# Kernel optimization log

Hardware: AMD Instinct MI355X
Metric: run time of the kernel (lower is better)

Reference implementation:

```python
import jax, jax.numpy as jnp
import numpy as np

B, N, D, R = 4, 50000, 64, 500
E_PER = 62500
E = B * E_PER


def _build_edges():
    rng = np.random.default_rng(0)
    idx = np.repeat(np.arange(B), E_PER)
    vi = rng.integers(0, N, E)
    vj = rng.integers(0, N, E)
    order = np.lexsort((vj, vi, idx))
    idx, vi, vj = idx[order], vi[order], vj[order]
    rel = rng.integers(0, R, E)
    key_vi = idx.astype(np.int64) * N + vi
    _, idx_vi = np.unique(key_vi, return_inverse=True)  # sorted -> nondecreasing segment ids
    key_vj = idx.astype(np.int64) * N + vj
    _, idx_vj = np.unique(key_vj, return_inverse=True)
    all_keys = np.concatenate([key_vi, key_vj])
    uniq_all, inv = np.unique(all_keys, return_inverse=True)
    e2vi, e2vj = inv[:E], inv[E:]
    sel = np.stack([idx, vi, vj, rel, idx_vi, idx_vj, e2vi, e2vj], axis=1).astype(np.int32)
    return sel, int(idx_vi.max() + 1), int(idx_vj.max() + 1), int(len(uniq_all))


def setup_inputs() -> dict:
    sel, n_vi_seg, n_vj_seg, n_visited = _build_edges()
    key = jax.random.key(0)
    ks = jax.random.split(key, 9)
    na = jax.random.uniform(ks[0], (B, N), jnp.float32) + 1e-6
    na = na / jnp.sum(na, axis=1, keepdims=True)
    return {
        'node_attention': na,
        'selected_edges': jnp.asarray(sel),
        'edges_y': jax.random.uniform(ks[1], (E,), jnp.float32, 0.1, 1.0),
        'hidden_con': jax.random.normal(ks[2], (n_visited, D), jnp.float32) * 0.1,
        'hidden_uncon': jax.random.normal(ks[3], (1, N, D), jnp.float32) * 0.1,
        'rel_emb': jax.random.normal(ks[4], (R, D), jnp.float32) * 0.1,
        'ws': jax.random.normal(ks[5], (8, D), jnp.float32) * (1.0 / np.sqrt(8.0)),
        'b': jax.random.normal(ks[6], (D,), jnp.float32) * 0.01,
        'out_w': jax.random.normal(ks[7], (D,), jnp.float32) * 0.3,
        'out_b': jax.random.normal(ks[8], (D,), jnp.float32) * 0.01,
        'n_vi_seg': n_vi_seg,
        'n_vj_seg': n_vj_seg,
    }


def reference(node_attention, selected_edges, edges_y, hidden_con, hidden_uncon,
              rel_emb, ws, b, out_w, out_b, n_vi_seg, n_vj_seg):
    idx, vi, vj = selected_edges[:, 0], selected_edges[:, 1], selected_edges[:, 2]
    rel, idx_vi, idx_vj = selected_edges[:, 3], selected_edges[:, 4], selected_edges[:, 5]
    e2vi, e2vj = selected_edges[:, 6], selected_edges[:, 7]

    # Node2Edge gathers
    hc_vi, hc_vj = hidden_con[e2vi], hidden_con[e2vj]        # [E, D]
    hu = hidden_uncon[0]                                     # hidden_uncon has batch 1
    hu_vi, hu_vj = hu[vi], hu[vj]                            # [E, D]
    re = rel_emb[rel]                                        # [E, D]

    # F layer: interact = [[0,3],[0,2,3],[0,4],[0,2,4],[1,3],[1,2,3],[1,4],[1,2,4]]
    terms = (hc_vi * hc_vj, hc_vi * re * hc_vj, hc_vi * hu_vj, hc_vi * re * hu_vj,
             hu_vi * hc_vj, hu_vi * re * hc_vj, hu_vi * hu_vj, hu_vi * re * hu_vj)
    f = b
    for k in range(8):
        f = f + ws[k] * terms[k]
    f = jax.nn.relu(f) * out_w + out_b                       # [E, D]
    logits = jnp.sum(f, axis=1)                              # [E]

    # NeighborSoftmax at='vi' (segment softmax)
    seg_max = jax.ops.segment_max(logits, idx_vi, num_segments=n_vi_seg)
    e = jnp.exp(logits - seg_max[idx_vi])
    es = jax.ops.segment_sum(e, idx_vi, num_segments=n_vi_seg)
    transition = e / es[idx_vi]

    # attention flow
    na_e = node_attention[idx, vi]
    ta = na_e * transition * edges_y

    # Aggregate at='vj', sum, then scatter into (B, n_nodes)
    aggr = jax.ops.segment_sum(ta, idx_vj, num_segments=n_vj_seg)
    seg_idx = jax.ops.segment_max(idx, idx_vj, num_segments=n_vj_seg)
    seg_vj = jax.ops.segment_max(vj, idx_vj, num_segments=n_vj_seg)
    Bn, Nn = node_attention.shape
    new_att = jnp.zeros((Bn, Nn), node_attention.dtype).at[seg_idx, seg_vj].add(aggr)
    return new_att / jnp.sum(new_att, axis=1, keepdims=True)
```

## Files before the change

kernel.cpp:

```cpp
#include <hip/hip_runtime.h>
#include <math.h>

#define D 64
#define CH 256
#define HALO 32
#define WSZ (CH + HALO)
#define BT 512
#define NT ((WSZ + 63) / 64)

__global__ void k_zero(float4* __restrict__ out4, float* __restrict__ row_sum,
                       int BN4, int Bn)
{
    const int i = blockIdx.x * 256 + threadIdx.x;
    if (i < BN4) out4[i] = make_float4(0.f, 0.f, 0.f, 0.f);
    if (i < Bn) row_sum[i] = 0.f;
}

__device__ __forceinline__ float edge_logit(
    const float4 a, const float4 c, const float4 ui, const float4 uj,
    const float4 r, const float* Wf, const float* Bvf, const float* Owf)
{
    const float* ap = (const float*)&a;  const float* cp = (const float*)&c;
    const float* up = (const float*)&ui; const float* vp = (const float*)&uj;
    const float* rp = (const float*)&r;
    float acc = 0.f;
    #pragma unroll
    for (int k4 = 0; k4 < 4; ++k4) {
        const float hcvi = ap[k4], hcvj = cp[k4], huvi = up[k4], huvj = vp[k4], rr = rp[k4];
        const float hcr = hcvi * rr, hur = huvi * rr;
        float f = Bvf[k4];
        f += Wf[0*4+k4] * (hcvi * hcvj);
        f += Wf[1*4+k4] * (hcr  * hcvj);
        f += Wf[2*4+k4] * (hcvi * huvj);
        f += Wf[3*4+k4] * (hcr  * huvj);
        f += Wf[4*4+k4] * (huvi * hcvj);
        f += Wf[5*4+k4] * (hur  * hcvj);
        f += Wf[6*4+k4] * (huvi * huvj);
        f += Wf[7*4+k4] * (hur  * huvj);
        acc += fmaxf(f, 0.f) * Owf[k4];
    }
    return acc;
}

#define ISSUE(A0, UI0, R0, A1, UI1, R1, C0, UJ0, C1, UJ1, T)              \
    {                                                                     \
        const int jj0 = (T) * 64 + wv * 8 + g;                            \
        const int jj1 = jj0 + 4;                                          \
        const int jc0 = (jj0 < Wc) ? jj0 : (Wc - 1);                      \
        const int jc1 = (jj1 < Wc) ? jj1 : (Wc - 1);                      \
        A0  = hc4[(size_t)s_sel[jc0 * 8 + 6] * 16 + d16];                 \
        UI0 = hu4[(size_t)s_sel[jc0 * 8 + 1] * 16 + d16];                 \
        R0  = re4[(size_t)s_sel[jc0 * 8 + 3] * 16 + d16];                 \
        C0  = hc4[(size_t)s_sel[jc0 * 8 + 7] * 16 + d16];                 \
        UJ0 = hu4[(size_t)s_sel[jc0 * 8 + 2] * 16 + d16];                 \
        A1  = hc4[(size_t)s_sel[jc1 * 8 + 6] * 16 + d16];                 \
        UI1 = hu4[(size_t)s_sel[jc1 * 8 + 1] * 16 + d16];                 \
        R1  = re4[(size_t)s_sel[jc1 * 8 + 3] * 16 + d16];                 \
        C1  = hc4[(size_t)s_sel[jc1 * 8 + 7] * 16 + d16];                 \
        UJ1 = hu4[(size_t)s_sel[jc1 * 8 + 2] * 16 + d16];                 \
    }

#define COMPUTE(A0, UI0, R0, A1, UI1, R1, C0, UJ0, C1, UJ1, T)            \
    {                                                                     \
        const int jj0 = (T) * 64 + wv * 8 + g;                            \
        const int jj1 = jj0 + 4;                                          \
        const bool v0 = (jj0 < Wc);                                       \
        const bool v1 = (jj1 < Wc);                                       \
        const int jc0 = v0 ? jj0 : (Wc - 1);                              \
        const int jc1 = v1 ? jj1 : (Wc - 1);                              \
        float acc0 = edge_logit(A0, C0, UI0, UJ0, R0, Wf, Bvf, Owf);      \
        float acc1 = edge_logit(A1, C1, UI1, UJ1, R1, Wf, Bvf, Owf);      \
        _Pragma("unroll")                                                 \
        for (int off = 8; off > 0; off >>= 1) {                           \
            acc0 += __shfl_xor(acc0, off, 64);                            \
            acc1 += __shfl_xor(acc1, off, 64);                            \
        }                                                                 \
        if (d16 == 0) {                                                   \
            if (v0) { s_logit[jj0] = acc0; s_ivi[jj0] = s_sel[jc0 * 8 + 4]; } \
            if (v1) { s_logit[jj1] = acc1; s_ivi[jj1] = s_sel[jc1 * 8 + 4]; } \
        }                                                                 \
    }

#define SCHED_FENCE() __builtin_amdgcn_sched_barrier(0)

__global__ __launch_bounds__(BT) void k_fused(
    const int* __restrict__ sel, const float* __restrict__ hc,
    const float* __restrict__ hu, const float* __restrict__ re,
    const float* __restrict__ wsm, const float* __restrict__ bias,
    const float* __restrict__ out_w,
    const float* __restrict__ na, const float* __restrict__ edges_y,
    float* __restrict__ out, float* __restrict__ row_sum,
    int E, int N)
{
    __shared__ int   s_sel[WSZ * 8];
    __shared__ float s_logit[WSZ];
    __shared__ int   s_ivi[WSZ];
    __shared__ float s_row[8];

    const int b0 = blockIdx.x * CH;
    const int Wc = min(WSZ, E - b0);

    {
        const int nint = Wc * 8;
        const int* selw = sel + (size_t)b0 * 8;
        for (int i = threadIdx.x; i < nint; i += BT) s_sel[i] = selw[i];
    }
    if (threadIdx.x < 8) s_row[threadIdx.x] = 0.f;

    const int lane = threadIdx.x & 63;
    const int g    = lane >> 4;
    const int d16  = lane & 15;
    const int wv   = threadIdx.x >> 6;

    const float4* wsm4 = (const float4*)wsm;
    float4 Wk[8];
    #pragma unroll
    for (int k = 0; k < 8; ++k) Wk[k] = wsm4[k * 16 + d16];
    const float4 Bv = ((const float4*)bias)[d16];
    const float4 Ow = ((const float4*)out_w)[d16];
    const float* Wf  = (const float*)Wk;
    const float* Bvf = (const float*)&Bv;
    const float* Owf = (const float*)&Ow;

    const float4* hc4 = (const float4*)hc;
    const float4* hu4 = (const float4*)hu;
    const float4* re4 = (const float4*)re;

    __syncthreads();

    float4 nA0a, nUI0a, nR0a, nA1a, nUI1a, nR1a, fC0a, fUJ0a, fC1a, fUJ1a;
    float4 nA0b, nUI0b, nR0b, nA1b, nUI1b, nR1b, fC0b, fUJ0b, fC1b, fUJ1b;

    ISSUE(nA0a, nUI0a, nR0a, nA1a, nUI1a, nR1a, fC0a, fUJ0a, fC1a, fUJ1a, 0);
    SCHED_FENCE();

    int t = 0;
    #pragma unroll 1
    for (; t + 1 < NT; t += 2) {
        ISSUE(nA0b, nUI0b, nR0b, nA1b, nUI1b, nR1b, fC0b, fUJ0b, fC1b, fUJ1b, t + 1);
        SCHED_FENCE();
        COMPUTE(nA0a, nUI0a, nR0a, nA1a, nUI1a, nR1a, fC0a, fUJ0a, fC1a, fUJ1a, t);
        SCHED_FENCE();
        ISSUE(nA0a, nUI0a, nR0a, nA1a, nUI1a, nR1a, fC0a, fUJ0a, fC1a, fUJ1a, t + 2);
        SCHED_FENCE();
        COMPUTE(nA0b, nUI0b, nR0b, nA1b, nUI1b, nR1b, fC0b, fUJ0b, fC1b, fUJ1b, t + 1);
        SCHED_FENCE();
    }
    COMPUTE(nA0a, nUI0a, nR0a, nA1a, nUI1a, nR1a, fC0a, fUJ0a, fC1a, fUJ1a, NT - 1);

    __syncthreads();

    const int ivi_prev = (b0 > 0) ? sel[((size_t)b0 - 1) * 8 + 4] : -1;

    for (int j = threadIdx.x; j < Wc; j += BT) {
        const int myivi = s_ivi[j];

        int s = j;
        while (s > 0 && s_ivi[s - 1] == myivi) --s;
        const bool genuine = (s > 0) || (myivi != ivi_prev);
        if (!genuine || s >= CH) continue;

        int en = j + 1;
        while (en < Wc && s_ivi[en] == myivi) ++en;

        float m = s_logit[j];
        for (int i = s; i < en; ++i) m = fmaxf(m, s_logit[i]);
        float sum = 0.f;
        for (int i = s; i < en; ++i) sum += __expf(s_logit[i] - m);

        const int idx = s_sel[j * 8 + 0];
        const int vi  = s_sel[j * 8 + 1];
        const int vj  = s_sel[j * 8 + 2];
        const float ta = na[(size_t)idx * N + vi]
                       * (__expf(s_logit[j] - m) / sum) * edges_y[b0 + j];

        atomicAdd(out + (size_t)idx * N + vj, ta);
        atomicAdd(&s_row[idx & 7], ta);
    }

    __syncthreads();
    if (threadIdx.x < 8) {
        const float v = s_row[threadIdx.x];
        if (v != 0.f) atomicAdd(row_sum + threadIdx.x, v);
    }
}

__global__ void k_norm(float4* __restrict__ out, const float* __restrict__ row_sum, int N4) {
    const int col = blockIdx.x * blockDim.x + threadIdx.x;
    const int row = blockIdx.y;
    if (col < N4) {
        const float inv = 1.f / row_sum[row];
        const size_t i = (size_t)row * N4 + col;
        float4 v = out[i];
        v.x *= inv; v.y *= inv; v.z *= inv; v.w *= inv;
        out[i] = v;
    }
}

extern "C" void kernel_launch(void* const* d_in, const int* in_sizes, int n_in,
                              void* d_out, int out_size, void* d_ws, size_t ws_size,
                              hipStream_t stream)
{
    const float* na    = (const float*)d_in[0];
    const int*   sel   = (const int*)  d_in[1];
    const float* ey    = (const float*)d_in[2];
    const float* hc    = (const float*)d_in[3];
    const float* hu    = (const float*)d_in[4];
    const float* re    = (const float*)d_in[5];
    const float* wsm   = (const float*)d_in[6];
    const float* bias  = (const float*)d_in[7];
    const float* ow    = (const float*)d_in[8];

    float* out = (float*)d_out;

    const int E  = in_sizes[2];
    const int N  = in_sizes[4] / D;
    const int BN = in_sizes[0];
    const int Bn = BN / N;

    float* row_sum = (float*)d_ws;

    const int N4  = N / 4;
    const int BN4 = BN / 4;

    k_zero<<<(BN4 + 255) / 256, 256, 0, stream>>>((float4*)out, row_sum, BN4, Bn);

    const int nblk = (E + CH - 1) / CH;
    k_fused<<<nblk, BT, 0, stream>>>(sel, hc, hu, re, wsm, bias, ow,
                                     na, ey, out, row_sum, E, N);

    dim3 ngrid((N4 + 255) / 256, Bn);
    k_norm<<<ngrid, 256, 0, stream>>>((float4*)out, row_sum, N4);
}
```

Baseline: 159.7 us.

## Simplify edge loop, move weights to shared memory, shrink block and chunk

Removes the hand-pipelined double-buffered gather (ISSUE/COMPUTE with scheduling barriers). Each wave now processes one edge per 16-lane group per iteration and the weight, bias and out_w vectors are read from LDS instead of registers. Chunk size drops from 256 to 128 edges and block size from 512 to 256 threads, which lowers register pressure so more waves can be resident to hide gather latency. In exchange it loses explicit load/compute overlap and doubles the halo overhead relative to the chunk size.

```diff
diff --git a/kernel.cpp b/kernel.cpp
--- a/kernel.cpp
+++ b/kernel.cpp
@@ -2,11 +2,11 @@
 #include <math.h>
 
 #define D 64
-#define CH 256
+#define CH 128
 #define HALO 32
 #define WSZ (CH + HALO)
-#define BT 512
-#define NT ((WSZ + 63) / 64)
+#define BT 256
+#define NT (WSZ / 16)
 
 __global__ void k_zero(float4* __restrict__ out4, float* __restrict__ row_sum,
                        int BN4, int Bn)
@@ -15,73 +15,6 @@
     if (i < BN4) out4[i] = make_float4(0.f, 0.f, 0.f, 0.f);
     if (i < Bn) row_sum[i] = 0.f;
 }
-
-__device__ __forceinline__ float edge_logit(
-    const float4 a, const float4 c, const float4 ui, const float4 uj,
-    const float4 r, const float* Wf, const float* Bvf, const float* Owf)
-{
-    const float* ap = (const float*)&a;  const float* cp = (const float*)&c;
-    const float* up = (const float*)&ui; const float* vp = (const float*)&uj;
-    const float* rp = (const float*)&r;
-    float acc = 0.f;
-    #pragma unroll
-    for (int k4 = 0; k4 < 4; ++k4) {
-        const float hcvi = ap[k4], hcvj = cp[k4], huvi = up[k4], huvj = vp[k4], rr = rp[k4];
-        const float hcr = hcvi * rr, hur = huvi * rr;
-        float f = Bvf[k4];
-        f += Wf[0*4+k4] * (hcvi * hcvj);
-        f += Wf[1*4+k4] * (hcr  * hcvj);
-        f += Wf[2*4+k4] * (hcvi * huvj);
-        f += Wf[3*4+k4] * (hcr  * huvj);
-        f += Wf[4*4+k4] * (huvi * hcvj);
-        f += Wf[5*4+k4] * (hur  * hcvj);
-        f += Wf[6*4+k4] * (huvi * huvj);
-        f += Wf[7*4+k4] * (hur  * huvj);
-        acc += fmaxf(f, 0.f) * Owf[k4];
-    }
-    return acc;
-}
-
-#define ISSUE(A0, UI0, R0, A1, UI1, R1, C0, UJ0, C1, UJ1, T)              \
-    {                                                                     \
-        const int jj0 = (T) * 64 + wv * 8 + g;                            \
-        const int jj1 = jj0 + 4;                                          \
-        const int jc0 = (jj0 < Wc) ? jj0 : (Wc - 1);                      \
-        const int jc1 = (jj1 < Wc) ? jj1 : (Wc - 1);                      \
-        A0  = hc4[(size_t)s_sel[jc0 * 8 + 6] * 16 + d16];                 \
-        UI0 = hu4[(size_t)s_sel[jc0 * 8 + 1] * 16 + d16];                 \
-        R0  = re4[(size_t)s_sel[jc0 * 8 + 3] * 16 + d16];                 \
-        C0  = hc4[(size_t)s_sel[jc0 * 8 + 7] * 16 + d16];                 \
-        UJ0 = hu4[(size_t)s_sel[jc0 * 8 + 2] * 16 + d16];                 \
-        A1  = hc4[(size_t)s_sel[jc1 * 8 + 6] * 16 + d16];                 \
-        UI1 = hu4[(size_t)s_sel[jc1 * 8 + 1] * 16 + d16];                 \
-        R1  = re4[(size_t)s_sel[jc1 * 8 + 3] * 16 + d16];                 \
-        C1  = hc4[(size_t)s_sel[jc1 * 8 + 7] * 16 + d16];                 \
-        UJ1 = hu4[(size_t)s_sel[jc1 * 8 + 2] * 16 + d16];                 \
-    }
-
-#define COMPUTE(A0, UI0, R0, A1, UI1, R1, C0, UJ0, C1, UJ1, T)            \
-    {                                                                     \
-        const int jj0 = (T) * 64 + wv * 8 + g;                            \
-        const int jj1 = jj0 + 4;                                          \
-        const bool v0 = (jj0 < Wc);                                       \
-        const bool v1 = (jj1 < Wc);                                       \
-        const int jc0 = v0 ? jj0 : (Wc - 1);                              \
-        const int jc1 = v1 ? jj1 : (Wc - 1);                              \
-        float acc0 = edge_logit(A0, C0, UI0, UJ0, R0, Wf, Bvf, Owf);      \
-        float acc1 = edge_logit(A1, C1, UI1, UJ1, R1, Wf, Bvf, Owf);      \
-        _Pragma("unroll")                                                 \
-        for (int off = 8; off > 0; off >>= 1) {                           \
-            acc0 += __shfl_xor(acc0, off, 64);                            \
-            acc1 += __shfl_xor(acc1, off, 64);                            \
-        }                                                                 \
-        if (d16 == 0) {                                                   \
-            if (v0) { s_logit[jj0] = acc0; s_ivi[jj0] = s_sel[jc0 * 8 + 4]; } \
-            if (v1) { s_logit[jj1] = acc1; s_ivi[jj1] = s_sel[jc1 * 8 + 4]; } \
-        }                                                                 \
-    }
-
-#define SCHED_FENCE() __builtin_amdgcn_sched_barrier(0)
 
 __global__ __launch_bounds__(BT) void k_fused(
     const int* __restrict__ sel, const float* __restrict__ hc,
@@ -95,6 +28,9 @@
     __shared__ int   s_sel[WSZ * 8];
     __shared__ float s_logit[WSZ];
     __shared__ int   s_ivi[WSZ];
+    __shared__ float s_w[8 * D];
+    __shared__ float s_bv[D];
+    __shared__ float s_ow[D];
     __shared__ float s_row[8];
 
     const int b0 = blockIdx.x * CH;
@@ -104,23 +40,18 @@
         const int nint = Wc * 8;
         const int* selw = sel + (size_t)b0 * 8;
         for (int i = threadIdx.x; i < nint; i += BT) s_sel[i] = selw[i];
+        for (int i = threadIdx.x; i < 8 * D; i += BT) s_w[i] = wsm[i];
+        if (threadIdx.x < D) {
+            s_bv[threadIdx.x] = bias[threadIdx.x];
+            s_ow[threadIdx.x] = out_w[threadIdx.x];
+        }
+        if (threadIdx.x < 8) s_row[threadIdx.x] = 0.f;
     }
-    if (threadIdx.x < 8) s_row[threadIdx.x] = 0.f;
 
     const int lane = threadIdx.x & 63;
     const int g    = lane >> 4;
     const int d16  = lane & 15;
     const int wv   = threadIdx.x >> 6;
-
-    const float4* wsm4 = (const float4*)wsm;
-    float4 Wk[8];
-    #pragma unroll
-    for (int k = 0; k < 8; ++k) Wk[k] = wsm4[k * 16 + d16];
-    const float4 Bv = ((const float4*)bias)[d16];
-    const float4 Ow = ((const float4*)out_w)[d16];
-    const float* Wf  = (const float*)Wk;
-    const float* Bvf = (const float*)&Bv;
-    const float* Owf = (const float*)&Ow;
 
     const float4* hc4 = (const float4*)hc;
     const float4* hu4 = (const float4*)hu;
@@ -128,25 +59,52 @@
 
     __syncthreads();
 
-    float4 nA0a, nUI0a, nR0a, nA1a, nUI1a, nR1a, fC0a, fUJ0a, fC1a, fUJ1a;
-    float4 nA0b, nUI0b, nR0b, nA1b, nUI1b, nR1b, fC0b, fUJ0b, fC1b, fUJ1b;
+    #pragma unroll 1
+    for (int t = 0; t < NT; ++t) {
+        const int jj = t * 16 + wv * 4 + g;
+        const bool v = (jj < Wc);
+        const int jc = v ? jj : (Wc - 1);
 
-    ISSUE(nA0a, nUI0a, nR0a, nA1a, nUI1a, nR1a, fC0a, fUJ0a, fC1a, fUJ1a, 0);
-    SCHED_FENCE();
+        const int e2vi = s_sel[jc * 8 + 6];
+        const int vig  = s_sel[jc * 8 + 1];
+        const int rel  = s_sel[jc * 8 + 3];
+        const int e2vj = s_sel[jc * 8 + 7];
+        const int vjg  = s_sel[jc * 8 + 2];
 
-    int t = 0;
-    #pragma unroll 1
-    for (; t + 1 < NT; t += 2) {
-        ISSUE(nA0b, nUI0b, nR0b, nA1b, nUI1b, nR1b, fC0b, fUJ0b, fC1b, fUJ1b, t + 1);
-        SCHED_FENCE();
-        COMPUTE(nA0a, nUI0a, nR0a, nA1a, nUI1a, nR1a, fC0a, fUJ0a, fC1a, fUJ1a, t);
-        SCHED_FENCE();
-        ISSUE(nA0a, nUI0a, nR0a, nA1a, nUI1a, nR1a, fC0a, fUJ0a, fC1a, fUJ1a, t + 2);
-        SCHED_FENCE();
-        COMPUTE(nA0b, nUI0b, nR0b, nA1b, nUI1b, nR1b, fC0b, fUJ0b, fC1b, fUJ1b, t + 1);
-        SCHED_FENCE();
+        const float4 a  = hc4[(size_t)e2vi * 16 + d16];
+        const float4 ui = hu4[(size_t)vig  * 16 + d16];
+        const float4 r  = re4[(size_t)rel  * 16 + d16];
+        const float4 c  = hc4[(size_t)e2vj * 16 + d16];
+        const float4 uj = hu4[(size_t)vjg  * 16 + d16];
+
+        float4 ar, uir;
+        ar.x  = a.x  * r.x;  ar.y  = a.y  * r.y;  ar.z  = a.z  * r.z;  ar.w  = a.w  * r.w;
+        uir.x = ui.x * r.x;  uir.y = ui.y * r.y;  uir.z = ui.z * r.z;  uir.w = ui.w * r.w;
+
+        float4 f = *(const float4*)(s_bv + (d16 << 2));
+        #pragma unroll
+        for (int k = 0; k < 8; ++k) {
+            const float4 w = *(const float4*)(s_w + k * D + (d16 << 2));
+            const float4 p = (k & 4) ? ((k & 1) ? uir : ui) : ((k & 1) ? ar : a);
+            const float4 q = (k & 2) ? uj : c;
+            f.x += w.x * (p.x * q.x);
+            f.y += w.y * (p.y * q.y);
+            f.z += w.z * (p.z * q.z);
+            f.w += w.w * (p.w * q.w);
+        }
+        const float4 ow = *(const float4*)(s_ow + (d16 << 2));
+        float acc = fmaxf(f.x, 0.f) * ow.x + fmaxf(f.y, 0.f) * ow.y
+                  + fmaxf(f.z, 0.f) * ow.z + fmaxf(f.w, 0.f) * ow.w;
+
+        #pragma unroll
+        for (int off = 8; off > 0; off >>= 1)
+            acc += __shfl_xor(acc, off, 64);
+
+        if (d16 == 0 && v) {
+            s_logit[jj] = acc;
+            s_ivi[jj]   = s_sel[jc * 8 + 4];
+        }
     }
-    COMPUTE(nA0a, nUI0a, nR0a, nA1a, nUI1a, nR1a, fC0a, fUJ0a, fC1a, fUJ1a, NT - 1);
 
     __syncthreads();
 
```

New measurement: 164.5 us. 1.03x slower.
